# Kernel tuning notes

Hardware: AMD Instinct MI355X
Metric: run time of the kernel (lower is better)

The kernel has to match this reference:

```python
import jax, jax.numpy as jnp
import numpy as np

B, NQ, E, D = 64, 64, 1024, 768
NH, NP = 16, 4
GH = GW = 24
EPS = 1e-5


def _ln(x, g, b):
    m = jnp.mean(x, axis=-1, keepdims=True)
    v = jnp.mean((x - m) ** 2, axis=-1, keepdims=True)
    return (x - m) / jnp.sqrt(v + EPS) * g + b


def _lin_init(k, fan_in, shape_w, shape_b):
    kw, kb = jax.random.split(k)
    s = 1.0 / np.sqrt(fan_in)
    w = jax.random.uniform(kw, shape_w, minval=-s, maxval=s, dtype=jnp.float32)
    b = jax.random.uniform(kb, shape_b, minval=-s, maxval=s, dtype=jnp.float32)
    return w, b


def setup_inputs() -> dict:
    key = jax.random.key(0)
    ks = jax.random.split(key, 16)
    inp = {}
    inp['features'] = jax.random.normal(ks[0], (B, GH * GW, D), dtype=jnp.float32)
    inp['p1_w'], inp['p1_b'] = _lin_init(ks[1], D, (E, D), (E,))
    inp['p2_w'], inp['p2_b'] = _lin_init(ks[2], 4 * D, (E, 4 * D), (E,))
    inp['p3_w'], inp['p3_b'] = _lin_init(ks[3], 9 * D, (E, 9 * D), (E,))
    inp['query_emb'] = jax.random.normal(ks[4], (1, NQ, E), dtype=jnp.float32)
    inp['rg_w1'], inp['rg_b1'] = _lin_init(ks[5], E, (E, E), (E,))
    inp['rg_g'] = jnp.ones((E,), jnp.float32)
    inp['rg_b'] = jnp.zeros((E,), jnp.float32)
    inp['rg_w2'], inp['rg_b2'] = _lin_init(ks[6], E, (2, E), (2,))
    # sampling_offsets: weight init to 0, bias uniform(-0.1, 0.1) per the module
    inp['so_w'] = jnp.zeros((NH * NP * 2, E), jnp.float32)
    inp['so_b'] = jax.random.uniform(ks[7], (NH * NP * 2,), minval=-0.1, maxval=0.1, dtype=jnp.float32)
    inp['aw_w'], inp['aw_b'] = _lin_init(ks[8], E, (NH * NP, E), (NH * NP,))
    inp['vp_w'], inp['vp_b'] = _lin_init(ks[9], E, (E, E), (E,))
    inp['op_w'], inp['op_b'] = _lin_init(ks[10], E, (E, E), (E,))
    inp['fln_g'] = jnp.ones((E,), jnp.float32)
    inp['fln_b'] = jnp.zeros((E,), jnp.float32)
    inp['fin_w'], inp['fin_b'] = _lin_init(ks[11], E, (E, E), (E,))
    return inp


def reference(features, p1_w, p1_b, p2_w, p2_b, p3_w, p3_b, query_emb,
              rg_w1, rg_b1, rg_g, rg_b, rg_w2, rg_b2,
              so_w, so_b, aw_w, aw_b, vp_w, vp_b, op_w, op_b,
              fln_g, fln_b, fin_w, fin_b):
    Bn = features.shape[0]
    hd = E // NH
    x = features.reshape(Bn, GH, GW, D)

    # ---- multi-scale feature extraction (2x2 / 3x3 block concat to match 4D/9D projections) ----
    s1 = features @ p1_w.T + p1_b                                   # [B, GH*GW, E]
    s2in = x.reshape(Bn, GH // 2, 2, GW // 2, 2, D).transpose(0, 1, 3, 2, 4, 5)
    s2 = s2in.reshape(Bn, (GH // 2) * (GW // 2), 4 * D) @ p2_w.T + p2_b
    s3in = x.reshape(Bn, GH // 3, 3, GW // 3, 3, D).transpose(0, 1, 3, 2, 4, 5)
    s3 = s3in.reshape(Bn, (GH // 3) * (GW // 3), 9 * D) @ p3_w.T + p3_b
    levels = [(GH, GW), (GH // 2, GW // 2), (GH // 3, GW // 3)]

    # ---- reference points from learned queries ----
    q = jnp.broadcast_to(query_emb, (Bn, NQ, E))
    h = jax.nn.gelu(_ln(q @ rg_w1.T + rg_b1, rg_g, rg_b), approximate=False)
    rp = jax.nn.sigmoid(h @ rg_w2.T + rg_b2)                        # [B, NQ, 2] in (0,1)

    # ---- deformable attention ----
    value = jnp.concatenate([s1, s2, s3], axis=1) @ vp_w.T + vp_b   # [B, Lv_tot, E]
    value = value.reshape(Bn, -1, NH, hd)
    off = (q @ so_w.T + so_b).reshape(Bn, NQ, NH, NP, 2)
    aw = jax.nn.softmax((q @ aw_w.T + aw_b).reshape(Bn, NQ, NH, NP), axis=-1)

    out = jnp.zeros((Bn, NQ, E), value.dtype)
    start = 0
    for (Hs, Ws) in levels:
        Lv = Hs * Ws
        sp = jnp.clip(rp[:, :, None, None, :] + off, 0.0, 1.0)      # [B, NQ, NH, NP, 2]
        x0 = jnp.floor(sp[..., 0] * (Ws - 1)).astype(jnp.int32)
        y0 = jnp.floor(sp[..., 1] * (Hs - 1)).astype(jnp.int32)
        idx = y0 * Ws + x0                                          # [B, NQ, NH, NP]
        vl = value[:, start:start + Lv].transpose(0, 2, 1, 3)       # [B, NH, Lv, hd]
        idx2 = idx.transpose(0, 2, 1, 3).reshape(Bn, NH, NQ * NP)
        g = jnp.take_along_axis(vl, idx2[..., None], axis=2)        # [B, NH, NQ*NP, hd]
        g = g.reshape(Bn, NH, NQ, NP, hd)
        out = out + jnp.einsum('bhqpd,bqhp->bqhd', g, aw).reshape(Bn, NQ, E)
        start += Lv

    out = out @ op_w.T + op_b
    return _ln(out, fln_g, fln_b) @ fin_w.T + fin_b
```

## Files before the change

### kernel.cpp

```cpp
#include <hip/hip_runtime.h>
#include <math.h>

#define EE 1024
#define WWN 10752

typedef __attribute__((ext_vector_type(4))) float f4;
typedef __attribute__((ext_vector_type(4))) float f32x4;
typedef __attribute__((ext_vector_type(8))) __bf16 bf16x8;
typedef __attribute__((ext_vector_type(8))) unsigned short ushort8;
typedef __attribute__((ext_vector_type(4))) unsigned short us4;

__device__ __forceinline__ unsigned short f2b(float x) {
    unsigned int u = __float_as_uint(x);
    unsigned int r = (u + 0x7fffu + ((u >> 16) & 1u)) >> 16;
    return (unsigned short)r;
}
__device__ __forceinline__ float b2f(unsigned short u) {
    unsigned int v = ((unsigned int)u) << 16;
    return __uint_as_float(v);
}

#define GLOAD16(g, l) __builtin_amdgcn_global_load_lds( \
    (const __attribute__((address_space(1))) unsigned int*)(g), \
    (__attribute__((address_space(3))) unsigned int*)(l), 16, 0, 0)

template<int MODE, bool SPLIT, int KT>
__device__ __forceinline__ void gemm_body(
    unsigned short* __restrict__ AsB, unsigned short* __restrict__ BsB,
    const unsigned short* __restrict__ FEAT, const unsigned short* __restrict__ WW,
    const float* __restrict__ bias, void* __restrict__ outp,
    int by, int bx, int ktBase)
{
    constexpr int gw = (MODE == 1) ? 24 : (MODE == 2 ? 12 : 8);
    constexpr int Rl = gw * gw;
    constexpr int colOff = (MODE == 1) ? 0 : (MODE == 2 ? 768 : 3840);

    const int t = threadIdx.x;
    const int lane = t & 63;
    const int w = t >> 6;
    const int wm = w >> 2;
    const int wn = w & 3;
    const int m0 = by * 256, n0 = bx * 256;

    f32x4 acc[8][4] = {};

    const int srow = lane >> 3;
    const int sseg = lane & 7;
    const int sgx  = sseg ^ srow;
    int rbA[4];
#pragma unroll
    for (int g = 0; g < 4; ++g) {
        int gr = m0 + w * 32 + g * 8 + srow;
        if (MODE == 1) rbA[g] = gr;
        else {
            int b_ = gr / Rl, rl = gr - b_ * Rl;
            rbA[g] = b_ * 576 + (MODE * (rl / gw)) * 24 + MODE * (rl % gw);
        }
    }
    const unsigned short* gBbase = WW + (size_t)(n0 + w * 32 + srow) * WWN + colOff + sgx * 8;

    const int fr = lane & 15;
    const int kg = lane >> 4;
    const int kgx0 = kg ^ (fr & 7);
    const int kgx1 = kgx0 ^ 4;
    const int aOff0 = (wm * 128 + fr) * 64 + kgx0 * 8;
    const int aOff1 = (wm * 128 + fr) * 64 + kgx1 * 8;
    const int bOff0 = (wn * 64 + fr) * 64 + kgx0 * 8;
    const int bOff1 = (wn * 64 + fr) * 64 + kgx1 * 8;

    auto STAGE = [&](int buf, int ktl) {
        int kt = ktBase + ktl;
        int s = kt / 12;
        int within = (kt - s * 12) * 64;
        int add = 0;
        if (MODE == 2)      add = (s >> 1) * 24 + (s & 1);
        else if (MODE == 3) { int di = s / 3; add = di * 24 + (s - 3 * di); }
        unsigned short* Asb = AsB + buf * 16384;
        unsigned short* Bsb = BsB + buf * 16384;
#pragma unroll
        for (int g = 0; g < 4; ++g)
            GLOAD16(FEAT + (size_t)(rbA[g] + add) * 768 + within + sgx * 8,
                    Asb + (w * 32 + g * 8) * 64);
#pragma unroll
        for (int g = 0; g < 4; ++g)
            GLOAD16(gBbase + (size_t)(g * 8) * WWN + (size_t)kt * 64,
                    Bsb + (w * 32 + g * 8) * 64);
    };

    int cur = 0;
    STAGE(0, 0);

    for (int tt = 0; tt < KT; ++tt) {
        asm volatile("s_waitcnt vmcnt(0)" ::: "memory");
        __builtin_amdgcn_s_barrier();
        __builtin_amdgcn_sched_barrier(0);

        if (tt + 1 < KT) STAGE(cur ^ 1, tt + 1);
        __builtin_amdgcn_sched_barrier(0);

        const unsigned short* Asc = AsB + cur * 16384;
        const unsigned short* Bsc = BsB + cur * 16384;

        {
            bf16x8 bf[4], af[8];
#pragma unroll
            for (int j = 0; j < 4; ++j) bf[j] = *(const bf16x8*)(Bsc + bOff0 + j * 1024);
#pragma unroll
            for (int i = 0; i < 8; ++i) af[i] = *(const bf16x8*)(Asc + aOff0 + i * 1024);
            __builtin_amdgcn_s_setprio(1);
#pragma unroll
            for (int i = 0; i < 8; ++i)
#pragma unroll
                for (int j = 0; j < 4; ++j)
                    acc[i][j] = __builtin_amdgcn_mfma_f32_16x16x32_bf16(af[i], bf[j], acc[i][j], 0, 0, 0);
            __builtin_amdgcn_s_setprio(0);
        }
        __builtin_amdgcn_s_barrier();
        __builtin_amdgcn_sched_barrier(0);

        {
            bf16x8 bf[4], af[8];
#pragma unroll
            for (int j = 0; j < 4; ++j) bf[j] = *(const bf16x8*)(Bsc + bOff1 + j * 1024);
#pragma unroll
            for (int i = 0; i < 8; ++i) af[i] = *(const bf16x8*)(Asc + aOff1 + i * 1024);
            __builtin_amdgcn_s_setprio(1);
#pragma unroll
            for (int i = 0; i < 8; ++i)
#pragma unroll
                for (int j = 0; j < 4; ++j)
                    acc[i][j] = __builtin_amdgcn_mfma_f32_16x16x32_bf16(af[i], bf[j], acc[i][j], 0, 0, 0);
            __builtin_amdgcn_s_setprio(0);
        }
        cur ^= 1;
    }

#pragma unroll
    for (int i = 0; i < 8; ++i) {
#pragma unroll
        for (int r = 0; r < 4; ++r) {
            int m = m0 + wm * 128 + i * 16 + kg * 4 + r;
#pragma unroll
            for (int j = 0; j < 4; ++j) {
                int n = n0 + wn * 64 + j * 16 + fr;
                if (SPLIT) {
                    ((unsigned short*)outp)[(size_t)m * EE + n] = f2b(acc[i][j][r]);
                } else {
                    ((unsigned short*)outp)[(size_t)m * EE + n] = f2b(acc[i][j][r] + bias[n]);
                }
            }
        }
    }
}

__global__ __launch_bounds__(512, 2) void gemm_val_merged(
    const unsigned short* __restrict__ FEAT, const unsigned short* __restrict__ WW,
    const float* __restrict__ b1, unsigned short* __restrict__ VAL,
    unsigned short* __restrict__ PART2, unsigned short* __restrict__ PART3)
{
    __shared__ unsigned short As[2 * 256 * 64];
    __shared__ unsigned short Bs[2 * 256 * 64];

    int bid = blockIdx.x;
    if (bid < 256) {
        int s = ((bid & 7) << 5) | (bid >> 3);
        int z = s >> 6, r = s & 63;
        gemm_body<3, true, 27>(As, Bs, FEAT, WW, nullptr,
                               PART3 + (size_t)z * 4194304, r >> 2, r & 3, z * 27);
    } else if (bid < 688) {
        int j = bid - 256;
        int s = (j & 7) * 54 + (j >> 3);
        int z = s / 144, r = s - z * 144;
        gemm_body<2, true, 16>(As, Bs, FEAT, WW, nullptr,
                               PART2 + (size_t)z * 9437184, r >> 2, r & 3, z * 16);
    } else {
        int j = bid - 688;
        int s = (j & 7) * 72 + (j >> 3);
        gemm_body<1, false, 12>(As, Bs, FEAT, WW, b1, VAL, s >> 2, s & 3, 0);
    }
}

__global__ void gather_fused_kernel(const unsigned short* __restrict__ VAL,
                                    const unsigned short* __restrict__ P2,
                                    const unsigned short* __restrict__ P3,
                                    const float* __restrict__ b2, const float* __restrict__ b3,
                                    const float* __restrict__ awf, const int* __restrict__ idxv,
                                    unsigned short* __restrict__ out0)
{
    int idx = blockIdx.x * 256 + threadIdx.x;
    int d8 = idx & 7;
    int h  = (idx >> 3) & 15;
    int bq = idx >> 7;
    int b  = bq >> 6, q = bq & 63;
    int n0 = h * 64 + d8 * 8;
    float s[8] = {0.f};

#pragma unroll
    for (int p = 0; p < 4; ++p) {
        int row = idxv[((0 * 64 + q) * 16 + h) * 4 + p];
        float wgt = awf[(q * 16 + h) * 4 + p];
        ushort8 v = *(const ushort8*)(VAL + ((size_t)(b * 576 + row)) * 1024 + n0);
#pragma unroll
        for (int i = 0; i < 8; ++i) s[i] += wgt * b2f(v[i]);
    }

    float bias2[8];
#pragma unroll
    for (int i = 0; i < 8; ++i) bias2[i] = b2[n0 + i];
#pragma unroll
    for (int p = 0; p < 4; ++p) {
        int rl = idxv[((1 * 64 + q) * 16 + h) * 4 + p] - 576;
        float wgt = awf[(q * 16 + h) * 4 + p];
        size_t mo = ((size_t)(b * 144 + rl)) * 1024 + n0;
        ushort8 va = *(const ushort8*)(P2 + mo);
        ushort8 vb = *(const ushort8*)(P2 + 9437184 + mo);
        ushort8 vc = *(const ushort8*)(P2 + 2 * 9437184 + mo);
#pragma unroll
        for (int i = 0; i < 8; ++i)
            s[i] += wgt * (b2f(va[i]) + b2f(vb[i]) + b2f(vc[i]) + bias2[i]);
    }

    float bias3[8];
#pragma unroll
    for (int i = 0; i < 8; ++i) bias3[i] = b3[n0 + i];
#pragma unroll
    for (int p = 0; p < 4; ++p) {
        int rl = idxv[((2 * 64 + q) * 16 + h) * 4 + p] - 720;
        float wgt = awf[(q * 16 + h) * 4 + p];
        size_t mo = ((size_t)(b * 64 + rl)) * 1024 + n0;
        float a8[8] = {0.f};
#pragma unroll
        for (int k = 0; k < 4; ++k) {
            ushort8 v = *(const ushort8*)(P3 + (size_t)k * 4194304 + mo);
#pragma unroll
            for (int i = 0; i < 8; ++i) a8[i] += b2f(v[i]);
        }
#pragma unroll
        for (int i = 0; i < 8; ++i) s[i] += wgt * (a8[i] + bias3[i]);
    }

    ushort8 o;
#pragma unroll
    for (int i = 0; i < 8; ++i) o[i] = f2b(s[i]);
    *(ushort8*)(out0 + (size_t)bq * 1024 + n0) = o;
}

template<bool OB>
__global__ __launch_bounds__(256, 2) void gemm2w(
    const unsigned short* __restrict__ A, const unsigned short* __restrict__ Bw,
    const float* __restrict__ bias, void* __restrict__ Cv,
    int M, int N, int K)
{
    __shared__ unsigned short As[2][128 * 64];
    __shared__ unsigned short Bs[2][128 * 64];

    const int t = threadIdx.x;
    const int lane = t & 63;
    const int w = t >> 6;
    const int wm = w >> 1, wn = w & 1;

    int nwg = gridDim.x * gridDim.y;
    int bid = blockIdx.y * gridDim.x + blockIdx.x;
    int chunk = nwg >> 3;
    int swz = (bid & 7) * chunk + (bid >> 3);
    int by = swz / gridDim.x, bx = swz % gridDim.x;
    const int m0 = by * 128, n0 = bx * 128;

    f32x4 acc[4][4] = {};

    const int srow = lane >> 3;
    const int sseg = lane & 7;
    const int sgx  = sseg ^ srow;
    const unsigned short* gA = A + (size_t)(m0 + w * 32 + srow) * K + sgx * 8;
    const unsigned short* gB = Bw + (size_t)(n0 + w * 32 + srow) * K + sgx * 8;

    const int fr = lane & 15;
    const int kg = lane >> 4;
    const int kgx0 = kg ^ (fr & 7);
    const int kgx1 = kgx0 ^ 4;
    const int aOff0 = (wm * 64 + fr) * 64 + kgx0 * 8;
    const int aOff1 = (wm * 64 + fr) * 64 + kgx1 * 8;
    const int bOff0 = (wn * 64 + fr) * 64 + kgx0 * 8;
    const int bOff1 = (wn * 64 + fr) * 64 + kgx1 * 8;

    auto STAGE = [&](int buf, int kt) {
        size_t k0 = (size_t)kt * 64;
#pragma unroll
        for (int g = 0; g < 4; ++g)
            GLOAD16(gA + (size_t)(g * 8) * K + k0, &As[buf][(w * 32 + g * 8) * 64]);
#pragma unroll
        for (int g = 0; g < 4; ++g)
            GLOAD16(gB + (size_t)(g * 8) * K + k0, &Bs[buf][(w * 32 + g * 8) * 64]);
    };

    const int nt = K >> 6;
    int cur = 0;
    STAGE(0, 0);

    for (int tt = 0; tt < nt; ++tt) {
        asm volatile("s_waitcnt vmcnt(0)" ::: "memory");
        __builtin_amdgcn_s_barrier();
        __builtin_amdgcn_sched_barrier(0);

        if (tt + 1 < nt) STAGE(cur ^ 1, tt + 1);
        __builtin_amdgcn_sched_barrier(0);

        {
            bf16x8 bf[4], af[4];
#pragma unroll
            for (int j = 0; j < 4; ++j) bf[j] = *(const bf16x8*)(&Bs[cur][bOff0] + j * 1024);
#pragma unroll
            for (int i = 0; i < 4; ++i) af[i] = *(const bf16x8*)(&As[cur][aOff0] + i * 1024);
            __builtin_amdgcn_s_setprio(1);
#pragma unroll
            for (int i = 0; i < 4; ++i)
#pragma unroll
                for (int j = 0; j < 4; ++j)
                    acc[i][j] = __builtin_amdgcn_mfma_f32_16x16x32_bf16(af[i], bf[j], acc[i][j], 0, 0, 0);
            __builtin_amdgcn_s_setprio(0);
        }
        __builtin_amdgcn_s_barrier();
        __builtin_amdgcn_sched_barrier(0);

        {
            bf16x8 bf[4], af[4];
#pragma unroll
            for (int j = 0; j < 4; ++j) bf[j] = *(const bf16x8*)(&Bs[cur][bOff1] + j * 1024);
#pragma unroll
            for (int i = 0; i < 4; ++i) af[i] = *(const bf16x8*)(&As[cur][aOff1] + i * 1024);
            __builtin_amdgcn_s_setprio(1);
#pragma unroll
            for (int i = 0; i < 4; ++i)
#pragma unroll
                for (int j = 0; j < 4; ++j)
                    acc[i][j] = __builtin_amdgcn_mfma_f32_16x16x32_bf16(af[i], bf[j], acc[i][j], 0, 0, 0);
            __builtin_amdgcn_s_setprio(0);
        }
        cur ^= 1;
    }

#pragma unroll
    for (int i = 0; i < 4; ++i) {
#pragma unroll
        for (int r = 0; r < 4; ++r) {
            int m = m0 + wm * 64 + i * 16 + kg * 4 + r;
#pragma unroll
            for (int j = 0; j < 4; ++j) {
                int n = n0 + wn * 64 + j * 16 + fr;
                float v = acc[i][j][r];
                if (bias) v += bias[n];
                if (OB) ((unsigned short*)Cv)[(size_t)m * N + n] = f2b(v);
                else    ((float*)Cv)[(size_t)m * N + n] = v;
            }
        }
    }
}

__global__ void mega_head_kernel(
    const float* __restrict__ qe, const float* __restrict__ rg_w1, const float* __restrict__ rg_b1,
    double* __restrict__ h0,
    const float* __restrict__ so_w, const float* __restrict__ so_b,
    const float* __restrict__ aw_w, const float* __restrict__ aw_b,
    double* __restrict__ offv_g, double* __restrict__ logit_g,
    const float* __restrict__ feat, unsigned short* __restrict__ FEAT,
    const float* __restrict__ vpw, unsigned short* __restrict__ VPW,
    const float* __restrict__ opw, unsigned short* __restrict__ OPW,
    const float* __restrict__ finw, unsigned short* __restrict__ FINW,
    const float* __restrict__ p1, const float* __restrict__ p2,
    const float* __restrict__ p3, unsigned short* __restrict__ PT,
    const float* __restrict__ vp_b,
    const float* __restrict__ pb1, const float* __restrict__ pb2, const float* __restrict__ pb3,
    float* __restrict__ o1, float* __restrict__ o2, float* __restrict__ o3)
{
    __shared__ float tile[32][33];
    int B = blockIdx.x;
    if (B < 16384) {
        int o = B * 4 + (threadIdx.x >> 6);
        int lane = threadIdx.x & 63;
        int q = o >> 10, n = o & 1023;
        double s = 0.0;
        for (int k = lane; k < EE; k += 64)
            s += (double)qe[q * EE + k] * (double)rg_w1[(size_t)n * EE + k];
#pragma unroll
        for (int off = 32; off > 0; off >>= 1) s += __shfl_down(s, off, 64);
        if (lane == 0) h0[o] = s + (double)rg_b1[n];
    } else if (B < 19456) {
        int o = (B - 16384) * 4 + (threadIdx.x >> 6);
        int lane = threadIdx.x & 63;
        const float* wrow;
        double bias;
        int q;
        if (o < 8192) { q = o >> 7; int j = o & 127; wrow = so_w + (size_t)j * EE; bias = (double)so_b[j]; }
        else          { int r = o - 8192; q = r >> 6; int n = r & 63; wrow = aw_w + (size_t)n * EE; bias = (double)aw_b[n]; }
        double s = 0.0;
        for (int k = lane; k < EE; k += 64)
            s += (double)qe[q * EE + k] * (double)wrow[k];
#pragma unroll
        for (int off = 32; off > 0; off >>= 1) s += __shfl_down(s, off, 64);
        if (lane == 0) {
            if (o < 8192) offv_g[o] = s + bias;
            else          logit_g[o - 8192] = s + bias;
        }
    } else {
        int blk = B - 19456;
        if (blk < 15360) {
            const float* in; unsigned short* out;
            if (blk < 13824)       { in = feat; out = FEAT; }
            else if (blk < 14336)  { in = vpw;  out = VPW;  blk -= 13824; }
            else if (blk < 14848)  { in = opw;  out = OPW;  blk -= 14336; }
            else                   { in = finw; out = FINW; blk -= 14848; }
            size_t i = ((size_t)blk * 256 + threadIdx.x) * 8;
            f4 x = *(const f4*)(in + i);
            f4 y = *(const f4*)(in + i + 4);
            ushort8 o;
            o[0] = f2b(x[0]); o[1] = f2b(x[1]); o[2] = f2b(x[2]); o[3] = f2b(x[3]);
            o[4] = f2b(y[0]); o[5] = f2b(y[1]); o[6] = f2b(y[2]); o[7] = f2b(y[3]);
            *(ushort8*)(out + i) = o;
        } else if (blk < 26112) {
            int fl = blk - 15360;
            int bx = fl % 336, byy = fl / 336;
            const float* in; unsigned short* out; int C;
            if (bx < 24)       { in = p1; out = PT;                C = 768; }
            else if (bx < 120) { in = p2; out = PT + 768  * 1024;  C = 3072; bx -= 24; }
            else               { in = p3; out = PT + 3840 * 1024;  C = 6912; bx -= 120; }
            const int R = 1024;
            int c0 = bx * 32, r0 = byy * 32;
            int tx = threadIdx.x & 31, ty = threadIdx.x >> 5;
#pragma unroll
            for (int i = 0; i < 32; i += 8)
                tile[ty + i][tx] = in[(size_t)(r0 + ty + i) * C + c0 + tx];
            __syncthreads();
#pragma unroll
            for (int i = 0; i < 32; i += 8)
                out[(size_t)(c0 + ty + i) * R + r0 + tx] = f2b(tile[tx][ty + i]);
        } else {
            int b = blk - 26112;
            const float* pb; float* bout;
            if (b < 256)      { pb = pb1; bout = o1; }
            else if (b < 512) { pb = pb2; bout = o2; b -= 256; }
            else              { pb = pb3; bout = o3; b -= 512; }
            int e = b * 4 + (threadIdx.x >> 6);
            int lane = threadIdx.x & 63;
            float s = 0.f;
            for (int k = lane; k < EE; k += 64) s += vpw[(size_t)e * EE + k] * pb[k];
#pragma unroll
            for (int o = 32; o > 0; o >>= 1) s += __shfl_down(s, o, 64);
            if (lane == 0) bout[e] = s + vp_b[e];
        }
    }
}

__global__ void qfin_kernel(const double* __restrict__ h0, const float* __restrict__ g,
                            const float* __restrict__ bb, const float* __restrict__ w2,
                            const float* __restrict__ b2,
                            const double* __restrict__ offv_g, const double* __restrict__ logit_g,
                            float* __restrict__ awf, int* __restrict__ idxv)
{
    __shared__ double red[256];
    __shared__ double stats[2];
    __shared__ double hsh[1024];
    __shared__ double rps[2];
    int q = blockIdx.x, t = threadIdx.x;
    double x[4];
#pragma unroll
    for (int i = 0; i < 4; ++i) x[i] = h0[q * 1024 + t + i * 256];
    double s = x[0] + x[1] + x[2] + x[3];
    red[t] = s; __syncthreads();
    for (int o = 128; o; o >>= 1) { if (t < o) red[t] += red[t + o]; __syncthreads(); }
    if (t == 0) stats[0] = red[0] / 1024.0;
    __syncthreads();
    double mean = stats[0];
    double d = 0.0;
#pragma unroll
    for (int i = 0; i < 4; ++i) { double dd = x[i] - mean; d += dd * dd; }
    red[t] = d; __syncthreads();
    for (int o = 128; o; o >>= 1) { if (t < o) red[t] += red[t + o]; __syncthreads(); }
    if (t == 0) stats[1] = red[0] / 1024.0;
    __syncthreads();
    double inv = 1.0 / sqrt(stats[1] + 1e-5);
#pragma unroll
    for (int i = 0; i < 4; ++i) {
        int c = t + i * 256;
        double y = (x[i] - mean) * inv * (double)g[c] + (double)bb[c];
        hsh[c] = y * 0.5 * (1.0 + erf(y * 0.70710678118654752440));
    }
    __syncthreads();
    if (t < 128) {
        int r = t >> 6;
        int lane = t & 63;
        double sv = 0.0;
        for (int k = lane; k < EE; k += 64)
            sv += hsh[k] * (double)w2[r * 1024 + k];
#pragma unroll
        for (int off = 32; off > 0; off >>= 1) sv += __shfl_down(sv, off, 64);
        if (lane == 0) rps[r] = 1.0 / (1.0 + exp(-(sv + (double)b2[r])));
    }
    __syncthreads();
    if (t < 64) {
        int hh = t >> 2, p = t & 3;
        const double* logit = logit_g + q * 64;
        const double* offv  = offv_g + q * 128;
        double l0 = logit[hh * 4 + 0], l1 = logit[hh * 4 + 1];
        double l2 = logit[hh * 4 + 2], l3 = logit[hh * 4 + 3];
        double m = fmax(fmax(l0, l1), fmax(l2, l3));
        double den = exp(l0 - m) + exp(l1 - m) + exp(l2 - m) + exp(l3 - m);
        awf[(q * 16 + hh) * 4 + p] = (float)(exp(logit[hh * 4 + p] - m) / den);
        const int Wss[3] = {24, 12, 8};
        const int starts[3] = {0, 576, 720};
        double ox = offv[(hh * 4 + p) * 2 + 0], oy = offv[(hh * 4 + p) * 2 + 1];
        double rx = rps[0], ry = rps[1];
#pragma unroll
        for (int l = 0; l < 3; ++l) {
            int Ws = Wss[l];
            double sx = rx + ox; sx = sx < 0.0 ? 0.0 : (sx > 1.0 ? 1.0 : sx);
            double sy = ry + oy; sy = sy < 0.0 ? 0.0 : (sy > 1.0 ? 1.0 : sy);
            int x0 = (int)floor(sx * (double)(Ws - 1));
            int y0 = (int)floor(sy * (double)(Ws - 1));
            idxv[((l * 64 + q) * 16 + hh) * 4 + p] = starts[l] + y0 * Ws + x0;
        }
    }
}

__global__ void ln_b2b_kernel(const unsigned short* __restrict__ x, const float* __restrict__ g,
                              const float* __restrict__ bb, unsigned short* __restrict__ y)
{
    __shared__ float red[256];
    __shared__ float stats[2];
    int r = blockIdx.x, t = threadIdx.x;
    us4 v4 = *(const us4*)(x + (size_t)r * 1024 + t * 4);
    float v[4];
#pragma unroll
    for (int i = 0; i < 4; ++i) v[i] = b2f(v4[i]);
    float s = v[0] + v[1] + v[2] + v[3];
    red[t] = s; __syncthreads();
    for (int o = 128; o; o >>= 1) { if (t < o) red[t] += red[t + o]; __syncthreads(); }
    if (t == 0) stats[0] = red[0] / 1024.f;
    __syncthreads();
    float mean = stats[0];
    float d = 0.f;
#pragma unroll
    for (int i = 0; i < 4; ++i) { float dd = v[i] - mean; d += dd * dd; }
    red[t] = d; __syncthreads();
    for (int o = 128; o; o >>= 1) { if (t < o) red[t] += red[t + o]; __syncthreads(); }
    if (t == 0) stats[1] = red[0] / 1024.f;
    __syncthreads();
    float inv = 1.f / sqrtf(stats[1] + 1e-5f);
    us4 o4;
#pragma unroll
    for (int i = 0; i < 4; ++i) {
        int c = t * 4 + i;
        o4[i] = f2b((v[i] - mean) * inv * g[c] + bb[c]);
    }
    *(us4*)(y + (size_t)r * 1024 + t * 4) = o4;
}

extern "C" void kernel_launch(void* const* d_in, const int* in_sizes, int n_in,
                              void* d_out, int out_size, void* d_ws, size_t ws_size,
                              hipStream_t stream)
{
    const float* features  = (const float*)d_in[0];
    const float* p1_w      = (const float*)d_in[1];
    const float* p1_b      = (const float*)d_in[2];
    const float* p2_w      = (const float*)d_in[3];
    const float* p2_b      = (const float*)d_in[4];
    const float* p3_w      = (const float*)d_in[5];
    const float* p3_b      = (const float*)d_in[6];
    const float* query_emb = (const float*)d_in[7];
    const float* rg_w1     = (const float*)d_in[8];
    const float* rg_b1     = (const float*)d_in[9];
    const float* rg_g      = (const float*)d_in[10];
    const float* rg_b      = (const float*)d_in[11];
    const float* rg_w2     = (const float*)d_in[12];
    const float* rg_b2     = (const float*)d_in[13];
    const float* so_w      = (const float*)d_in[14];
    const float* so_b      = (const float*)d_in[15];
    const float* aw_w      = (const float*)d_in[16];
    const float* aw_b      = (const float*)d_in[17];
    const float* vp_w      = (const float*)d_in[18];
    const float* vp_b      = (const float*)d_in[19];
    const float* op_w      = (const float*)d_in[20];
    const float* op_b      = (const float*)d_in[21];
    const float* fln_g     = (const float*)d_in[22];
    const float* fln_b     = (const float*)d_in[23];
    const float* fin_w     = (const float*)d_in[24];
    const float* fin_b     = (const float*)d_in[25];
    float* out = (float*)d_out;

    char* p = (char*)d_ws;
    unsigned short* FEAT = (unsigned short*)p; p += 56623104;
    unsigned short* PT   = (unsigned short*)p; p += 22020096;
    unsigned short* WW   = (unsigned short*)p; p += 22020096;
    unsigned short* VPW  = (unsigned short*)p; p += 2097152;
    unsigned short* VAL  = (unsigned short*)p; p += 75497472;
    unsigned short* PART = (unsigned short*)p; p += 90177536;
    unsigned short* OPO  = (unsigned short*)p; p += 8388608;
    unsigned short* OUT0 = (unsigned short*)p; p += 8388608;
    unsigned short* LNO  = (unsigned short*)p; p += 8388608;
    unsigned short* OPW  = (unsigned short*)p; p += 2097152;
    unsigned short* FINW = (unsigned short*)p; p += 2097152;
    float* b1p  = (float*)p; p += 4096;
    float* b2p  = (float*)p; p += 4096;
    float* b3p  = (float*)p; p += 4096;
    float* awf  = (float*)p; p += 16384;
    int*   idxv = (int*)p;   p += 49152;
    double* h0  = (double*)p; p += 524288;
    double* offv_g  = (double*)p; p += 65536;
    double* logit_g = (double*)p; p += 32768;

    unsigned short* PART2 = PART;
    unsigned short* PART3 = PART + 3 * 9437184;

    dim3 blk(256);

    mega_head_kernel<<<46336, blk, 0, stream>>>(
        query_emb, rg_w1, rg_b1, h0,
        so_w, so_b, aw_w, aw_b, offv_g, logit_g,
        features, FEAT, vp_w, VPW, op_w, OPW, fin_w, FINW,
        p1_w, p2_w, p3_w, PT,
        vp_b, p1_b, p2_b, p3_b, b1p, b2p, b3p);

    qfin_kernel<<<64, blk, 0, stream>>>(h0, rg_g, rg_b, rg_w2, rg_b2,
                                        offv_g, logit_g, awf, idxv);

    gemm2w<true><<<dim3(84, 8), blk, 0, stream>>>(VPW, PT, nullptr, WW, 1024, WWN, 1024);

    gemm_val_merged<<<1264, 512, 0, stream>>>(FEAT, WW, b1p, VAL, PART2, PART3);

    gather_fused_kernel<<<2048, blk, 0, stream>>>(VAL, PART2, PART3, b2p, b3p, awf, idxv, OUT0);

    gemm2w<true><<<dim3(8, 32), blk, 0, stream>>>(OUT0, OPW, op_b, OPO, 4096, 1024, 1024);
    ln_b2b_kernel<<<4096, blk, 0, stream>>>(OPO, fln_g, fln_b, LNO);
    gemm2w<false><<<dim3(8, 32), blk, 0, stream>>>(LNO, FINW, fin_b, out, 4096, 1024, 1024);
}
```

Baseline: 436.5 us.

## Split-K final GEMMs, merge qfin into WW GEMM launch, fuse partial sums into LN

The small qfin kernel now runs as extra blocks inside the WW weight-product GEMM launch, which removes one launch and lets the two overlap. The op_proj and final 4096x1024x1024 GEMMs use split-K=2 with fp32 partials, raising the grid from 256 to 512 blocks to fill more CUs. The partial sums are reduced inside the LayerNorm kernel together with the op bias, and a new reduction kernel handles the final output. This adds extra fp32 partial traffic and one more small kernel in exchange for better occupancy.

```diff
diff --git a/kernel.cpp b/kernel.cpp
--- a/kernel.cpp
+++ b/kernel.cpp
@@ -246,24 +246,16 @@
 }
 
 template<bool OB>
-__global__ __launch_bounds__(256, 2) void gemm2w(
+__device__ __forceinline__ void gemm2w_body(
+    unsigned short* __restrict__ AsB, unsigned short* __restrict__ BsB,
     const unsigned short* __restrict__ A, const unsigned short* __restrict__ Bw,
     const float* __restrict__ bias, void* __restrict__ Cv,
-    int M, int N, int K)
-{
-    __shared__ unsigned short As[2][128 * 64];
-    __shared__ unsigned short Bs[2][128 * 64];
-
+    int M, int N, int K, int by, int bx, int kBase, int nt)
+{
     const int t = threadIdx.x;
     const int lane = t & 63;
     const int w = t >> 6;
     const int wm = w >> 1, wn = w & 1;
-
-    int nwg = gridDim.x * gridDim.y;
-    int bid = blockIdx.y * gridDim.x + blockIdx.x;
-    int chunk = nwg >> 3;
-    int swz = (bid & 7) * chunk + (bid >> 3);
-    int by = swz / gridDim.x, bx = swz % gridDim.x;
     const int m0 = by * 128, n0 = bx * 128;
 
     f32x4 acc[4][4] = {};
@@ -271,8 +263,8 @@
     const int srow = lane >> 3;
     const int sseg = lane & 7;
     const int sgx  = sseg ^ srow;
-    const unsigned short* gA = A + (size_t)(m0 + w * 32 + srow) * K + sgx * 8;
-    const unsigned short* gB = Bw + (size_t)(n0 + w * 32 + srow) * K + sgx * 8;
+    const unsigned short* gA = A + (size_t)(m0 + w * 32 + srow) * K + kBase + sgx * 8;
+    const unsigned short* gB = Bw + (size_t)(n0 + w * 32 + srow) * K + kBase + sgx * 8;
 
     const int fr = lane & 15;
     const int kg = lane >> 4;
@@ -285,15 +277,16 @@
 
     auto STAGE = [&](int buf, int kt) {
         size_t k0 = (size_t)kt * 64;
+        unsigned short* Asb = AsB + buf * 8192;
+        unsigned short* Bsb = BsB + buf * 8192;
 #pragma unroll
         for (int g = 0; g < 4; ++g)
-            GLOAD16(gA + (size_t)(g * 8) * K + k0, &As[buf][(w * 32 + g * 8) * 64]);
+            GLOAD16(gA + (size_t)(g * 8) * K + k0, Asb + (w * 32 + g * 8) * 64);
 #pragma unroll
         for (int g = 0; g < 4; ++g)
-            GLOAD16(gB + (size_t)(g * 8) * K + k0, &Bs[buf][(w * 32 + g * 8) * 64]);
+            GLOAD16(gB + (size_t)(g * 8) * K + k0, Bsb + (w * 32 + g * 8) * 64);
     };
 
-    const int nt = K >> 6;
     int cur = 0;
     STAGE(0, 0);
 
@@ -305,12 +298,15 @@
         if (tt + 1 < nt) STAGE(cur ^ 1, tt + 1);
         __builtin_amdgcn_sched_barrier(0);
 
+        const unsigned short* Asc = AsB + cur * 8192;
+        const unsigned short* Bsc = BsB + cur * 8192;
+
         {
             bf16x8 bf[4], af[4];
 #pragma unroll
-            for (int j = 0; j < 4; ++j) bf[j] = *(const bf16x8*)(&Bs[cur][bOff0] + j * 1024);
-#pragma unroll
-            for (int i = 0; i < 4; ++i) af[i] = *(const bf16x8*)(&As[cur][aOff0] + i * 1024);
+            for (int j = 0; j < 4; ++j) bf[j] = *(const bf16x8*)(Bsc + bOff0 + j * 1024);
+#pragma unroll
+            for (int i = 0; i < 4; ++i) af[i] = *(const bf16x8*)(Asc + aOff0 + i * 1024);
             __builtin_amdgcn_s_setprio(1);
 #pragma unroll
             for (int i = 0; i < 4; ++i)
@@ -325,9 +321,9 @@
         {
             bf16x8 bf[4], af[4];
 #pragma unroll
-            for (int j = 0; j < 4; ++j) bf[j] = *(const bf16x8*)(&Bs[cur][bOff1] + j * 1024);
-#pragma unroll
-            for (int i = 0; i < 4; ++i) af[i] = *(const bf16x8*)(&As[cur][aOff1] + i * 1024);
+            for (int j = 0; j < 4; ++j) bf[j] = *(const bf16x8*)(Bsc + bOff1 + j * 1024);
+#pragma unroll
+            for (int i = 0; i < 4; ++i) af[i] = *(const bf16x8*)(Asc + aOff1 + i * 1024);
             __builtin_amdgcn_s_setprio(1);
 #pragma unroll
             for (int i = 0; i < 4; ++i)
@@ -354,6 +350,167 @@
             }
         }
     }
+}
+
+__device__ __forceinline__ void qfin_body(
+    int q, double* red, double* stats, double* hsh, double* rps,
+    const double* __restrict__ h0, const float* __restrict__ g,
+    const float* __restrict__ bb, const float* __restrict__ w2,
+    const float* __restrict__ b2,
+    const double* __restrict__ offv_g, const double* __restrict__ logit_g,
+    float* __restrict__ awf, int* __restrict__ idxv)
+{
+    int t = threadIdx.x;
+    double x[4];
+#pragma unroll
+    for (int i = 0; i < 4; ++i) x[i] = h0[q * 1024 + t + i * 256];
+    double s = x[0] + x[1] + x[2] + x[3];
+    red[t] = s; __syncthreads();
+    for (int o = 128; o; o >>= 1) { if (t < o) red[t] += red[t + o]; __syncthreads(); }
+    if (t == 0) stats[0] = red[0] / 1024.0;
+    __syncthreads();
+    double mean = stats[0];
+    double d = 0.0;
+#pragma unroll
+    for (int i = 0; i < 4; ++i) { double dd = x[i] - mean; d += dd * dd; }
+    red[t] = d; __syncthreads();
+    for (int o = 128; o; o >>= 1) { if (t < o) red[t] += red[t + o]; __syncthreads(); }
+    if (t == 0) stats[1] = red[0] / 1024.0;
+    __syncthreads();
+    double inv = 1.0 / sqrt(stats[1] + 1e-5);
+#pragma unroll
+    for (int i = 0; i < 4; ++i) {
+        int c = t + i * 256;
+        double y = (x[i] - mean) * inv * (double)g[c] + (double)bb[c];
+        hsh[c] = y * 0.5 * (1.0 + erf(y * 0.70710678118654752440));
+    }
+    __syncthreads();
+    if (t < 128) {
+        int r = t >> 6;
+        int lane = t & 63;
+        double sv = 0.0;
+        for (int k = lane; k < EE; k += 64)
+            sv += hsh[k] * (double)w2[r * 1024 + k];
+#pragma unroll
+        for (int off = 32; off > 0; off >>= 1) sv += __shfl_down(sv, off, 64);
+        if (lane == 0) rps[r] = 1.0 / (1.0 + exp(-(sv + (double)b2[r])));
+    }
+    __syncthreads();
+    if (t < 64) {
+        int hh = t >> 2, p = t & 3;
+        const double* logit = logit_g + q * 64;
+        const double* offv  = offv_g + q * 128;
+        double l0 = logit[hh * 4 + 0], l1 = logit[hh * 4 + 1];
+        double l2 = logit[hh * 4 + 2], l3 = logit[hh * 4 + 3];
+        double m = fmax(fmax(l0, l1), fmax(l2, l3));
+        double den = exp(l0 - m) + exp(l1 - m) + exp(l2 - m) + exp(l3 - m);
+        awf[(q * 16 + hh) * 4 + p] = (float)(exp(logit[hh * 4 + p] - m) / den);
+        const int Wss[3] = {24, 12, 8};
+        const int starts[3] = {0, 576, 720};
+        double ox = offv[(hh * 4 + p) * 2 + 0], oy = offv[(hh * 4 + p) * 2 + 1];
+        double rx = rps[0], ry = rps[1];
+#pragma unroll
+        for (int l = 0; l < 3; ++l) {
+            int Ws = Wss[l];
+            double sx = rx + ox; sx = sx < 0.0 ? 0.0 : (sx > 1.0 ? 1.0 : sx);
+            double sy = ry + oy; sy = sy < 0.0 ? 0.0 : (sy > 1.0 ? 1.0 : sy);
+            int x0 = (int)floor(sx * (double)(Ws - 1));
+            int y0 = (int)floor(sy * (double)(Ws - 1));
+            idxv[((l * 64 + q) * 16 + hh) * 4 + p] = starts[l] + y0 * Ws + x0;
+        }
+    }
+}
+
+__global__ __launch_bounds__(256, 2) void ww_qfin_kernel(
+    const unsigned short* __restrict__ VPW, const unsigned short* __restrict__ PT,
+    unsigned short* __restrict__ WW,
+    const double* __restrict__ h0, const float* __restrict__ rg_g,
+    const float* __restrict__ rg_b, const float* __restrict__ rg_w2,
+    const float* __restrict__ rg_b2,
+    const double* __restrict__ offv_g, const double* __restrict__ logit_g,
+    float* __restrict__ awf, int* __restrict__ idxv)
+{
+    __shared__ unsigned short As[2 * 128 * 64];
+    __shared__ unsigned short Bs[2 * 128 * 64];
+    __shared__ double qsh[256 + 2 + 1024 + 2];
+
+    int bid = blockIdx.x;
+    if (bid < 672) {
+        int swz = (bid & 7) * 84 + (bid >> 3);
+        int by = swz / 84, bx = swz % 84;
+        gemm2w_body<true>(As, Bs, VPW, PT, nullptr, WW, 1024, WWN, 1024, by, bx, 0, 16);
+    } else {
+        qfin_body(bid - 672, qsh, qsh + 256, qsh + 258, qsh + 1282,
+                  h0, rg_g, rg_b, rg_w2, rg_b2, offv_g, logit_g, awf, idxv);
+    }
+}
+
+__global__ __launch_bounds__(256, 2) void gemm_pk_kernel(
+    const unsigned short* __restrict__ A, const unsigned short* __restrict__ Bw,
+    float* __restrict__ P)
+{
+    __shared__ unsigned short As[2 * 128 * 64];
+    __shared__ unsigned short Bs[2 * 128 * 64];
+    int nwg = gridDim.x * gridDim.y;
+    int bid = blockIdx.y * gridDim.x + blockIdx.x;
+    int chunk = nwg >> 3;
+    int swz = (bid & 7) * chunk + (bid >> 3);
+    int by = swz / gridDim.x, bx = swz % gridDim.x;
+    gemm2w_body<false>(As, Bs, A, Bw, nullptr,
+                       P + (size_t)blockIdx.z * 4194304,
+                       4096, 1024, 1024, by, bx, blockIdx.z * 512, 8);
+}
+
+__global__ void lnsum_b2b_kernel(const float* __restrict__ p0, const float* __restrict__ p1,
+                                 const float* __restrict__ opb, const float* __restrict__ g,
+                                 const float* __restrict__ bb, unsigned short* __restrict__ y)
+{
+    __shared__ float red[256];
+    __shared__ float stats[2];
+    int r = blockIdx.x, t = threadIdx.x;
+    f4 a = *(const f4*)(p0 + (size_t)r * 1024 + t * 4);
+    f4 bvec = *(const f4*)(p1 + (size_t)r * 1024 + t * 4);
+    float v[4];
+#pragma unroll
+    for (int i = 0; i < 4; ++i) v[i] = a[i] + bvec[i] + opb[t * 4 + i];
+    float s = v[0] + v[1] + v[2] + v[3];
+    red[t] = s; __syncthreads();
+    for (int o = 128; o; o >>= 1) { if (t < o) red[t] += red[t + o]; __syncthreads(); }
+    if (t == 0) stats[0] = red[0] / 1024.f;
+    __syncthreads();
+    float mean = stats[0];
+    float d = 0.f;
+#pragma unroll
+    for (int i = 0; i < 4; ++i) { float dd = v[i] - mean; d += dd * dd; }
+    red[t] = d; __syncthreads();
+    for (int o = 128; o; o >>= 1) { if (t < o) red[t] += red[t + o]; __syncthreads(); }
+    if (t == 0) stats[1] = red[0] / 1024.f;
+    __syncthreads();
+    float inv = 1.f / sqrtf(stats[1] + 1e-5f);
+    us4 o4;
+#pragma unroll
+    for (int i = 0; i < 4; ++i) {
+        int c = t * 4 + i;
+        o4[i] = f2b((v[i] - mean) * inv * g[c] + bb[c]);
+    }
+    *(us4*)(y + (size_t)r * 1024 + t * 4) = o4;
+}
+
+__global__ void finred_kernel(const float* __restrict__ p0, const float* __restrict__ p1,
+                              const float* __restrict__ fb, float* __restrict__ out)
+{
+    int idx = blockIdx.x * 256 + threadIdx.x;
+    size_t e0 = (size_t)idx * 8;
+    int n = (int)(e0 & 1023);
+    f4 a0 = *(const f4*)(p0 + e0);
+    f4 a1 = *(const f4*)(p0 + e0 + 4);
+    f4 b0 = *(const f4*)(p1 + e0);
+    f4 b1 = *(const f4*)(p1 + e0 + 4);
+    f4 o0, o1;
+#pragma unroll
+    for (int i = 0; i < 4; ++i) { o0[i] = a0[i] + b0[i] + fb[n + i]; o1[i] = a1[i] + b1[i] + fb[n + 4 + i]; }
+    *(f4*)(out + e0) = o0;
+    *(f4*)(out + e0 + 4) = o1;
 }
 
 __global__ void mega_head_kernel(
@@ -448,110 +605,6 @@
             if (lane == 0) bout[e] = s + vp_b[e];
         }
     }
-}
-
-__global__ void qfin_kernel(const double* __restrict__ h0, const float* __restrict__ g,
-                            const float* __restrict__ bb, const float* __restrict__ w2,
-                            const float* __restrict__ b2,
-                            const double* __restrict__ offv_g, const double* __restrict__ logit_g,
-                            float* __restrict__ awf, int* __restrict__ idxv)
-{
-    __shared__ double red[256];
-    __shared__ double stats[2];
-    __shared__ double hsh[1024];
-    __shared__ double rps[2];
-    int q = blockIdx.x, t = threadIdx.x;
-    double x[4];
-#pragma unroll
-    for (int i = 0; i < 4; ++i) x[i] = h0[q * 1024 + t + i * 256];
-    double s = x[0] + x[1] + x[2] + x[3];
-    red[t] = s; __syncthreads();
-    for (int o = 128; o; o >>= 1) { if (t < o) red[t] += red[t + o]; __syncthreads(); }
-    if (t == 0) stats[0] = red[0] / 1024.0;
-    __syncthreads();
-    double mean = stats[0];
-    double d = 0.0;
-#pragma unroll
-    for (int i = 0; i < 4; ++i) { double dd = x[i] - mean; d += dd * dd; }
-    red[t] = d; __syncthreads();
-    for (int o = 128; o; o >>= 1) { if (t < o) red[t] += red[t + o]; __syncthreads(); }
-    if (t == 0) stats[1] = red[0] / 1024.0;
-    __syncthreads();
-    double inv = 1.0 / sqrt(stats[1] + 1e-5);
-#pragma unroll
-    for (int i = 0; i < 4; ++i) {
-        int c = t + i * 256;
-        double y = (x[i] - mean) * inv * (double)g[c] + (double)bb[c];
-        hsh[c] = y * 0.5 * (1.0 + erf(y * 0.70710678118654752440));
-    }
-    __syncthreads();
-    if (t < 128) {
-        int r = t >> 6;
-        int lane = t & 63;
-        double sv = 0.0;
-        for (int k = lane; k < EE; k += 64)
-            sv += hsh[k] * (double)w2[r * 1024 + k];
-#pragma unroll
-        for (int off = 32; off > 0; off >>= 1) sv += __shfl_down(sv, off, 64);
-        if (lane == 0) rps[r] = 1.0 / (1.0 + exp(-(sv + (double)b2[r])));
-    }
-    __syncthreads();
-    if (t < 64) {
-        int hh = t >> 2, p = t & 3;
-        const double* logit = logit_g + q * 64;
-        const double* offv  = offv_g + q * 128;
-        double l0 = logit[hh * 4 + 0], l1 = logit[hh * 4 + 1];
-        double l2 = logit[hh * 4 + 2], l3 = logit[hh * 4 + 3];
-        double m = fmax(fmax(l0, l1), fmax(l2, l3));
-        double den = exp(l0 - m) + exp(l1 - m) + exp(l2 - m) + exp(l3 - m);
-        awf[(q * 16 + hh) * 4 + p] = (float)(exp(logit[hh * 4 + p] - m) / den);
-        const int Wss[3] = {24, 12, 8};
-        const int starts[3] = {0, 576, 720};
-        double ox = offv[(hh * 4 + p) * 2 + 0], oy = offv[(hh * 4 + p) * 2 + 1];
-        double rx = rps[0], ry = rps[1];
-#pragma unroll
-        for (int l = 0; l < 3; ++l) {
-            int Ws = Wss[l];
-            double sx = rx + ox; sx = sx < 0.0 ? 0.0 : (sx > 1.0 ? 1.0 : sx);
-            double sy = ry + oy; sy = sy < 0.0 ? 0.0 : (sy > 1.0 ? 1.0 : sy);
-            int x0 = (int)floor(sx * (double)(Ws - 1));
-            int y0 = (int)floor(sy * (double)(Ws - 1));
-            idxv[((l * 64 + q) * 16 + hh) * 4 + p] = starts[l] + y0 * Ws + x0;
-        }
-    }
-}
-
-__global__ void ln_b2b_kernel(const unsigned short* __restrict__ x, const float* __restrict__ g,
-                              const float* __restrict__ bb, unsigned short* __restrict__ y)
-{
-    __shared__ float red[256];
-    __shared__ float stats[2];
-    int r = blockIdx.x, t = threadIdx.x;
-    us4 v4 = *(const us4*)(x + (size_t)r * 1024 + t * 4);
-    float v[4];
-#pragma unroll
-    for (int i = 0; i < 4; ++i) v[i] = b2f(v4[i]);
-    float s = v[0] + v[1] + v[2] + v[3];
-    red[t] = s; __syncthreads();
-    for (int o = 128; o; o >>= 1) { if (t < o) red[t] += red[t + o]; __syncthreads(); }
-    if (t == 0) stats[0] = red[0] / 1024.f;
-    __syncthreads();
-    float mean = stats[0];
-    float d = 0.f;
-#pragma unroll
-    for (int i = 0; i < 4; ++i) { float dd = v[i] - mean; d += dd * dd; }
-    red[t] = d; __syncthreads();
-    for (int o = 128; o; o >>= 1) { if (t < o) red[t] += red[t + o]; __syncthreads(); }
-    if (t == 0) stats[1] = red[0] / 1024.f;
-    __syncthreads();
-    float inv = 1.f / sqrtf(stats[1] + 1e-5f);
-    us4 o4;
-#pragma unroll
-    for (int i = 0; i < 4; ++i) {
-        int c = t * 4 + i;
-        o4[i] = f2b((v[i] - mean) * inv * g[c] + bb[c]);
-    }
-    *(us4*)(y + (size_t)r * 1024 + t * 4) = o4;
 }
 
 extern "C" void kernel_launch(void* const* d_in, const int* in_sizes, int n_in,
@@ -593,7 +646,6 @@
     unsigned short* VPW  = (unsigned short*)p; p += 2097152;
     unsigned short* VAL  = (unsigned short*)p; p += 75497472;
     unsigned short* PART = (unsigned short*)p; p += 90177536;
-    unsigned short* OPO  = (unsigned short*)p; p += 8388608;
     unsigned short* OUT0 = (unsigned short*)p; p += 8388608;
     unsigned short* LNO  = (unsigned short*)p; p += 8388608;
     unsigned short* OPW  = (unsigned short*)p; p += 2097152;
@@ -609,6 +661,7 @@
 
     unsigned short* PART2 = PART;
     unsigned short* PART3 = PART + 3 * 9437184;
+    float* PPK = (float*)PART;
 
     dim3 blk(256);
 
@@ -619,16 +672,17 @@
         p1_w, p2_w, p3_w, PT,
         vp_b, p1_b, p2_b, p3_b, b1p, b2p, b3p);
 
-    qfin_kernel<<<64, blk, 0, stream>>>(h0, rg_g, rg_b, rg_w2, rg_b2,
-                                        offv_g, logit_g, awf, idxv);
-
-    gemm2w<true><<<dim3(84, 8), blk, 0, stream>>>(VPW, PT, nullptr, WW, 1024, WWN, 1024);
+    ww_qfin_kernel<<<736, blk, 0, stream>>>(VPW, PT, WW,
+                                            h0, rg_g, rg_b, rg_w2, rg_b2,
+                                            offv_g, logit_g, awf, idxv);
 
     gemm_val_merged<<<1264, 512, 0, stream>>>(FEAT, WW, b1p, VAL, PART2, PART3);
 
     gather_fused_kernel<<<2048, blk, 0, stream>>>(VAL, PART2, PART3, b2p, b3p, awf, idxv, OUT0);
 
-    gemm2w<true><<<dim3(8, 32), blk, 0, stream>>>(OUT0, OPW, op_b, OPO, 4096, 1024, 1024);
-    ln_b2b_kernel<<<4096, blk, 0, stream>>>(OPO, fln_g, fln_b, LNO);
-    gemm2w<false><<<dim3(8, 32), blk, 0, stream>>>(LNO, FINW, fin_b, out, 4096, 1024, 1024);
-}
+    gemm_pk_kernel<<<dim3(8, 32, 2), blk, 0, stream>>>(OUT0, OPW, PPK);
+    lnsum_b2b_kernel<<<4096, blk, 0, stream>>>(PPK, PPK + 4194304, op_b, fln_g, fln_b, LNO);
+
+    gemm_pk_kernel<<<dim3(8, 32, 2), blk, 0, stream>>>(LNO, FINW, PPK);
+    finred_kernel<<<2048, blk, 0, stream>>>(PPK, PPK + 4194304, fin_b, out);
+}
```

Result: faster. 410.8 us (-5.9%).
